# Optimization experiments

Hardware: AMD Instinct MI355X
Metric: run time of the kernel (lower is better)

Reference implementation:

```python
import jax, jax.numpy as jnp
import numpy as np

BOX = 32  # uniform ROI crop size (y1-y0 = x1-x0 = 32)


def setup_inputs() -> dict:
    key = jax.random.key(0)
    k1, k2, k3 = jax.random.split(key, 3)
    B, C, H, W = 8, 256, 200, 200
    N = 512
    feature_map = jax.random.normal(k1, (B, C, H, W), dtype=jnp.float32)
    boxes_yx = jax.random.randint(k2, (N, 2), 0, H - BOX, dtype=jnp.int32)  # top-left (y0, x0)
    assoc = jax.random.randint(k3, (N,), 0, B, dtype=jnp.int32)            # sample index per box
    return {"feature_map": feature_map, "boxes_yx": boxes_yx, "assoc": assoc}


def reference(feature_map, boxes_yx, assoc):
    # Faithful RoiCut: for each box i, crop feature_map[assoc[i], :, y0:y0+BOX, x0:x0+BOX].
    # clip_boxes=True -> clip box coords into the scene extent.
    B, C, H, W = feature_map.shape
    yx = jnp.clip(boxes_yx, 0, jnp.array([H - BOX, W - BOX], dtype=boxes_yx.dtype))

    def crop(a, yx_i):
        fm = feature_map[a]  # [C, H, W] gather of the associated sample
        return jax.lax.dynamic_slice(fm, (jnp.int32(0), yx_i[0], yx_i[1]), (C, BOX, BOX))

    box_features = jax.vmap(crop)(assoc, yx)  # [N, C, BOX, BOX]
    return box_features
```

## Files before the change

kernel.cpp:

```cpp
#include <hip/hip_runtime.h>


constexpr int C_   = 256;
constexpr int H_   = 200;
constexpr int W_   = 200;
constexpr int BOX_ = 32;
constexpr int N_   = 512;

__global__ __launch_bounds__(512) void sort_boxes_kernel(
    const int* __restrict__ boxes,
    const int* __restrict__ assoc,
    int*       __restrict__ perm)
{
    __shared__ unsigned int key[N_];
    int t = threadIdx.x;

    int y0 = boxes[2 * t];
    int x0 = boxes[2 * t + 1];
    y0 = min(max(y0, 0), H_ - BOX_);
    x0 = min(max(x0, 0), W_ - BOX_);
    unsigned int a = (unsigned int)assoc[t];
    key[t] = (a << 25) | ((unsigned int)y0 << 17) | ((unsigned int)x0 << 9) | (unsigned int)t;
    __syncthreads();

    for (int k = 2; k <= N_; k <<= 1) {
        for (int j = k >> 1; j > 0; j >>= 1) {
            int ixj = t ^ j;
            if (ixj > t) {
                unsigned int va = key[t], vb = key[ixj];
                bool asc = ((t & k) == 0);
                if ((va > vb) == asc) { key[t] = vb; key[ixj] = va; }
            }
            __syncthreads();
        }
    }

    perm[t] = (int)(key[t] & 511u);
}

__global__ __launch_bounds__(256) void roicut_kernel(
    const float* __restrict__ fm,
    const int*   __restrict__ boxes,
    const int*   __restrict__ assoc,
    const int*   __restrict__ perm,
    float*       __restrict__ out)
{
    int b = blockIdx.x;
    int s = b >> 8;
    int c = b & 255;
    int t = threadIdx.x;

    int i  = perm[s];
    int a  = assoc[i];
    int y0 = boxes[2 * i];
    int x0 = boxes[2 * i + 1];
    y0 = min(max(y0, 0), H_ - BOX_);
    x0 = min(max(x0, 0), W_ - BOX_);

    int y = t >> 3;
    int x = (t & 7) << 2;

    const float* src = fm + ((((size_t)a * C_ + c) * H_ + (y0 + y)) * W_ + (x0 + x));
    float4 v;
    v.x = src[0];
    v.y = src[1];
    v.z = src[2];
    v.w = src[3];

    float* dst = out + (((size_t)i << 18) | (unsigned)(c << 10) | (unsigned)(t << 2));
    *reinterpret_cast<float4*>(dst) = v;
}

extern "C" void kernel_launch(void* const* d_in, const int* in_sizes, int n_in,
                              void* d_out, int out_size, void* d_ws, size_t ws_size,
                              hipStream_t stream) {
    const float* fm    = (const float*)d_in[0];
    const int*   boxes = (const int*)d_in[1];
    const int*   assoc = (const int*)d_in[2];
    float*       out   = (float*)d_out;
    int*         perm  = (int*)d_ws;

    sort_boxes_kernel<<<1, N_, 0, stream>>>(boxes, assoc, perm);

    int grid = N_ * C_;
    roicut_kernel<<<grid, 256, 0, stream>>>(fm, boxes, assoc, perm, out);
}
```

Measured before the change: 202.4 us.

## Process four channels per block, reorder grid by box, use nontemporal stores

Each block now copies four channels of one box instead of one, which cuts the grid by a factor of four and issues four independent loads per thread before the stores. The block index is remapped so consecutive blocks walk the sorted boxes at a fixed channel group rather than walking channels of one box. Output writes use nontemporal stores to keep the write-once output out of the cache. The reordering changes cache locality across overlapping boxes, which could help or hurt.

```diff
diff --git a/kernel.cpp b/kernel.cpp
--- a/kernel.cpp
+++ b/kernel.cpp
@@ -1,11 +1,14 @@
 #include <hip/hip_runtime.h>
 
+
+typedef float v4f __attribute__((ext_vector_type(4)));
 
 constexpr int C_   = 256;
 constexpr int H_   = 200;
 constexpr int W_   = 200;
 constexpr int BOX_ = 32;
 constexpr int N_   = 512;
+constexpr int CPB_ = 4;
 
 __global__ __launch_bounds__(512) void sort_boxes_kernel(
     const int* __restrict__ boxes,
@@ -46,8 +49,8 @@
     float*       __restrict__ out)
 {
     int b = blockIdx.x;
-    int s = b >> 8;
-    int c = b & 255;
+    int s = b & (N_ - 1);
+    int g = b >> 9;
     int t = threadIdx.x;
 
     int i  = perm[s];
@@ -60,15 +63,23 @@
     int y = t >> 3;
     int x = (t & 7) << 2;
 
-    const float* src = fm + ((((size_t)a * C_ + c) * H_ + (y0 + y)) * W_ + (x0 + x));
-    float4 v;
-    v.x = src[0];
-    v.y = src[1];
-    v.z = src[2];
-    v.w = src[3];
+    int c0 = g * CPB_;
+    const float* src0 = fm + ((((size_t)a * C_ + c0) * H_ + (y0 + y)) * W_ + (x0 + x));
+    float*       dst0 = out + (((size_t)i << 18) + ((size_t)c0 << 10) + ((size_t)t << 2));
 
-    float* dst = out + (((size_t)i << 18) | (unsigned)(c << 10) | (unsigned)(t << 2));
-    *reinterpret_cast<float4*>(dst) = v;
+    v4f v[CPB_];
+    #pragma unroll
+    for (int j = 0; j < CPB_; ++j) {
+        const float* src = src0 + (size_t)j * (H_ * W_);
+        v[j][0] = src[0];
+        v[j][1] = src[1];
+        v[j][2] = src[2];
+        v[j][3] = src[3];
+    }
+    #pragma unroll
+    for (int j = 0; j < CPB_; ++j) {
+        __builtin_nontemporal_store(v[j], reinterpret_cast<v4f*>(dst0 + (j << 10)));
+    }
 }
 
 extern "C" void kernel_launch(void* const* d_in, const int* in_sizes, int n_in,
@@ -82,6 +93,6 @@
 
     sort_boxes_kernel<<<1, N_, 0, stream>>>(boxes, assoc, perm);
 
-    int grid = N_ * C_;
+    int grid = N_ * (C_ / CPB_);
     roicut_kernel<<<grid, 256, 0, stream>>>(fm, boxes, assoc, perm, out);
 }
```

Result: slower. 215.7 us (+6.6%).

## Stage whole channel planes in LDS and emit all sample box crops

Applied to the files above, without the earlier changes.

Each block now handles one (sample, channel) plane: it copies the full 200x200 plane into LDS, then writes every box crop for that sample from LDS. The sort kernel now also produces per-sample start offsets, so each block knows which boxes it serves. The aim is to read each input plane from HBM once instead of re-reading overlapping crop regions, and output writes use nontemporal stores. The cost is a huge LDS footprint, about 160KB per block, which allows only one block per CU with no overlap between the load and store phases. Work per block also becomes uneven because samples hold different numbers of boxes.

```diff
diff --git a/kernel.cpp b/kernel.cpp
--- a/kernel.cpp
+++ b/kernel.cpp
@@ -1,16 +1,22 @@
 #include <hip/hip_runtime.h>
 
 
-constexpr int C_   = 256;
-constexpr int H_   = 200;
-constexpr int W_   = 200;
-constexpr int BOX_ = 32;
-constexpr int N_   = 512;
+typedef float v4f __attribute__((ext_vector_type(4)));
+
+constexpr int C_    = 256;
+constexpr int H_    = 200;
+constexpr int W_    = 200;
+constexpr int BOX_  = 32;
+constexpr int N_    = 512;
+constexpr int B_    = 8;
+constexpr int PLANE  = H_ * W_;
+constexpr int PLANE4 = PLANE / 4;
 
 __global__ __launch_bounds__(512) void sort_boxes_kernel(
     const int* __restrict__ boxes,
     const int* __restrict__ assoc,
-    int*       __restrict__ perm)
+    unsigned int* __restrict__ keys,
+    int* __restrict__ starts)
 {
     __shared__ unsigned int key[N_];
     int t = threadIdx.x;
@@ -35,40 +41,76 @@
         }
     }
 
-    perm[t] = (int)(key[t] & 511u);
+    unsigned int v = key[t];
+    keys[t] = v;
+    int at = (int)(v >> 25);
+    int ap = (t == 0) ? -1 : (int)(key[t - 1] >> 25);
+    for (int aa = ap + 1; aa <= at; ++aa) starts[aa] = t;
+    if (t == N_ - 1) for (int aa = at + 1; aa <= B_; ++aa) starts[aa] = N_;
 }
 
-__global__ __launch_bounds__(256) void roicut_kernel(
+__global__ __launch_bounds__(1024) void roicut_kernel(
     const float* __restrict__ fm,
-    const int*   __restrict__ boxes,
-    const int*   __restrict__ assoc,
-    const int*   __restrict__ perm,
-    float*       __restrict__ out)
+    const unsigned int* __restrict__ keys,
+    const int* __restrict__ starts,
+    float* __restrict__ out)
 {
-    int b = blockIdx.x;
-    int s = b >> 8;
-    int c = b & 255;
+    extern __shared__ float lds[];
+
+    int bid = blockIdx.x;
+    int a = bid >> 8;
+    int c = bid & 255;
     int t = threadIdx.x;
 
-    int i  = perm[s];
-    int a  = assoc[i];
-    int y0 = boxes[2 * i];
-    int x0 = boxes[2 * i + 1];
-    y0 = min(max(y0, 0), H_ - BOX_);
-    x0 = min(max(x0, 0), W_ - BOX_);
+    const v4f* src = (const v4f*)(fm + (size_t)(a * C_ + c) * PLANE);
+    v4f* l4 = (v4f*)lds;
+    v4f r0 = src[t];
+    v4f r1 = src[t + 1024];
+    v4f r2 = src[t + 2048];
+    v4f r3 = src[t + 3072];
+    v4f r4 = src[t + 4096];
+    v4f r5 = src[t + 5120];
+    v4f r6 = src[t + 6144];
+    v4f r7 = src[t + 7168];
+    v4f r8 = src[t + 8192];
+    bool tail = (t + 9216) < PLANE4;
+    v4f r9;
+    if (tail) r9 = src[t + 9216];
+    l4[t]        = r0;
+    l4[t + 1024] = r1;
+    l4[t + 2048] = r2;
+    l4[t + 3072] = r3;
+    l4[t + 4096] = r4;
+    l4[t + 5120] = r5;
+    l4[t + 6144] = r6;
+    l4[t + 7168] = r7;
+    l4[t + 8192] = r8;
+    if (tail) l4[t + 9216] = r9;
+    __syncthreads();
 
-    int y = t >> 3;
-    int x = (t & 7) << 2;
+    int b0 = starts[a], b1 = starts[a + 1];
+    int sub = t >> 8;
+    int q   = t & 255;
+    int y   = q >> 3;
+    int xg  = (q & 7) << 2;
 
-    const float* src = fm + ((((size_t)a * C_ + c) * H_ + (y0 + y)) * W_ + (x0 + x));
-    float4 v;
-    v.x = src[0];
-    v.y = src[1];
-    v.z = src[2];
-    v.w = src[3];
-
-    float* dst = out + (((size_t)i << 18) | (unsigned)(c << 10) | (unsigned)(t << 2));
-    *reinterpret_cast<float4*>(dst) = v;
+    for (int b = b0; b < b1; b += 4) {
+        int bb = b + sub;
+        if (bb < b1) {
+            unsigned int v = keys[bb];
+            int y0 = (v >> 17) & 255;
+            int x0 = (v >> 9) & 255;
+            int i  = (int)(v & 511u);
+            const float* p = lds + (y0 + y) * W_ + (x0 + xg);
+            v4f vv;
+            vv[0] = p[0];
+            vv[1] = p[1];
+            vv[2] = p[2];
+            vv[3] = p[3];
+            v4f* dst = (v4f*)(out + (((size_t)i << 18) + ((size_t)c << 10) + (size_t)(q << 2)));
+            __builtin_nontemporal_store(vv, dst);
+        }
+    }
 }
 
 extern "C" void kernel_launch(void* const* d_in, const int* in_sizes, int n_in,
@@ -78,10 +120,16 @@
     const int*   boxes = (const int*)d_in[1];
     const int*   assoc = (const int*)d_in[2];
     float*       out   = (float*)d_out;
-    int*         perm  = (int*)d_ws;
 
-    sort_boxes_kernel<<<1, N_, 0, stream>>>(boxes, assoc, perm);
+    unsigned int* keys   = (unsigned int*)d_ws;
+    int*          starts = (int*)d_ws + N_;
 
-    int grid = N_ * C_;
-    roicut_kernel<<<grid, 256, 0, stream>>>(fm, boxes, assoc, perm, out);
+    (void)hipFuncSetAttribute((const void*)roicut_kernel,
+                              hipFuncAttributeMaxDynamicSharedMemorySize,
+                              PLANE * (int)sizeof(float));
+
+    sort_boxes_kernel<<<1, N_, 0, stream>>>(boxes, assoc, keys, starts);
+
+    int grid = B_ * C_;
+    roicut_kernel<<<grid, 1024, PLANE * sizeof(float), stream>>>(fm, keys, starts, out);
 }
```

Result: faster. 173.4 us (-14.4%).
